# Kernel tuning notes

Measured on AMD Instinct MI355X. Metric: run time of the kernel, lower is better.

## Reference

```python
import jax, jax.numpy as jnp
import numpy as np

B, S, D, H = 2, 2048, 768, 12
HD = D // H
WINDOW = 64  # local_attention // 2
ROPE_THETA = 10000.0
NEG = -1e9


def setup_inputs() -> dict:
    key = jax.random.key(0)
    k1, k2, k3 = jax.random.split(key, 3)
    hidden_states = jax.random.normal(k1, (B, S, D), dtype=jnp.float32)
    Wqkv_w = jax.random.normal(k2, (3 * D, D), dtype=jnp.float32) * (D ** -0.5)
    Wo_w = jax.random.normal(k3, (D, D), dtype=jnp.float32) * (D ** -0.5)
    position_ids = jnp.broadcast_to(jnp.arange(S, dtype=jnp.int64 if jax.config.jax_enable_x64 else jnp.int32), (B, S))
    # additive sliding-window mask: 0 inside window, -1e9 outside (matches torch ModernBert mask construction)
    idx = np.arange(S)
    dist = np.abs(idx[:, None] - idx[None, :])
    sliding_window_mask = jnp.asarray(np.where(dist <= WINDOW, 0.0, NEG), dtype=jnp.float32)[None, None]  # [1,1,S,S]
    return {"hidden_states": hidden_states, "Wqkv_w": Wqkv_w, "Wo_w": Wo_w,
            "sliding_window_mask": sliding_window_mask, "position_ids": position_ids}


def _rotate_half(x):
    x1, x2 = jnp.split(x, 2, axis=-1)
    return jnp.concatenate([-x2, x1], axis=-1)


def reference(hidden_states, Wqkv_w, Wo_w, sliding_window_mask, position_ids):
    b, s, d = hidden_states.shape
    qkv = hidden_states @ Wqkv_w.T                      # [B,S,3D]
    qkv = qkv.reshape(b, s, 3, H, HD)
    q = qkv[:, :, 0].transpose(0, 2, 1, 3)              # [B,H,S,HD]
    k = qkv[:, :, 1].transpose(0, 2, 1, 3)
    v = qkv[:, :, 2].transpose(0, 2, 1, 3)
    # RoPE
    inv_freq = 1.0 / (ROPE_THETA ** (jnp.arange(0, HD, 2, dtype=jnp.float32) / HD))  # [HD/2]
    freqs = position_ids.astype(jnp.float32)[..., None] * inv_freq                   # [B,S,HD/2]
    emb = jnp.concatenate([freqs, freqs], axis=-1)                                   # [B,S,HD]
    cos = jnp.cos(emb)[:, None]                          # [B,1,S,HD]
    sin = jnp.sin(emb)[:, None]
    q = q * cos + _rotate_half(q) * sin
    k = k * cos + _rotate_half(k) * sin
    scale = HD ** -0.5
    scores = jnp.einsum('bhqd,bhkd->bhqk', q, k) * scale + sliding_window_mask       # [B,H,S,S]
    attn = jax.nn.softmax(scores.astype(jnp.float32), axis=-1).astype(q.dtype)
    out = jnp.einsum('bhqk,bhkd->bhqd', attn, v)         # [B,H,S,HD]
    out = out.transpose(0, 2, 1, 3).reshape(b, s, d)     # [B,S,D]
    return out @ Wo_w.T
```

## Files before the change

### kernel.cpp

```cpp
#include <hip/hip_runtime.h>
#include <hip/hip_bf16.h>
#include <cmath>

#define B_   2
#define S_   2048
#define D_   768
#define H_   12
#define HD_  64
#define WIN_ 64

typedef __bf16 bf16x8 __attribute__((ext_vector_type(8)));
typedef __bf16 bf16x4 __attribute__((ext_vector_type(4)));
typedef float  f32x4  __attribute__((ext_vector_type(4)));
typedef unsigned int u32;

__device__ __forceinline__ void async_ld16(const void* g, void* l) {
    __builtin_amdgcn_global_load_lds(
        (__attribute__((address_space(1))) void*)(size_t)g,
        (__attribute__((address_space(3))) void*)(u32)(size_t)l,
        16, 0, 0);
}

#define NHS (B_ * S_ * D_)
#define NWQ (3 * D_ * D_)
#define NWO (D_ * D_)

__global__ __launch_bounds__(256) void to_bf16_3(const float* __restrict__ a,
                                                 const float* __restrict__ b,
                                                 const float* __restrict__ c,
                                                 __bf16* __restrict__ oa,
                                                 __bf16* __restrict__ ob,
                                                 __bf16* __restrict__ oc) {
    const int NA = NHS / 4, NB = NWQ / 4;
    int v = blockIdx.x * 256 + threadIdx.x;
    const float* src; __bf16* dst; int idx;
    if (v < NA)           { src = a; dst = oa; idx = v; }
    else if (v < NA + NB) { src = b; dst = ob; idx = v - NA; }
    else                  { src = c; dst = oc; idx = v - NA - NB; }
    float4 x = ((const float4*)src)[idx];
    bf16x4 y = { (__bf16)x.x, (__bf16)x.y, (__bf16)x.z, (__bf16)x.w };
    *(bf16x4*)(dst + (size_t)idx * 4) = y;
}

#define BM 128
#define BN 128
#define BK 32

template <int MODE>
__global__ __launch_bounds__(256) void gemm_as(const __bf16* __restrict__ A,
                                               const __bf16* __restrict__ Bw,
                                               float* __restrict__ C,
                                               __bf16* __restrict__ qkv,
                                               __bf16* __restrict__ vt,
                                               int M, int N, int K) {
    __shared__ __attribute__((aligned(16))) __bf16 As[BM * BK];
    __shared__ __attribute__((aligned(16))) __bf16 Bs[BN * BK];

    const int tid  = threadIdx.x;
    const int m0   = blockIdx.y * BM;
    const int n0   = blockIdx.x * BN;
    const int w    = tid >> 6;
    const int lane = tid & 63;
    const int wm   = (w >> 1) * 64;
    const int wn   = (w & 1) * 64;
    const int fr   = lane & 15;
    const int fq   = lane >> 4;

    f32x4 acc[4][4] = {};

    for (int k0 = 0; k0 < K; k0 += BK) {
        #pragma unroll
        for (int i = 0; i < 2; ++i) {
            int c = i * 256 + tid;
            int row = c >> 2, cc = c & 3;
            async_ld16(A  + (size_t)(m0 + row) * K + k0 + cc * 8, As + c * 8);
            async_ld16(Bw + (size_t)(n0 + row) * K + k0 + cc * 8, Bs + c * 8);
        }
        __syncthreads();

        bf16x8 af[4], bfv[4];
        #pragma unroll
        for (int t = 0; t < 4; ++t) {
            af[t]  = *(const bf16x8*)(As + (wm + t * 16 + fr) * BK + fq * 8);
            bfv[t] = *(const bf16x8*)(Bs + (wn + t * 16 + fr) * BK + fq * 8);
        }
        #pragma unroll
        for (int ti = 0; ti < 4; ++ti)
            #pragma unroll
            for (int tj = 0; tj < 4; ++tj)
                acc[ti][tj] = __builtin_amdgcn_mfma_f32_16x16x32_bf16(
                    af[ti], bfv[tj], acc[ti][tj], 0, 0, 0);

        __syncthreads();
    }

    if (MODE == 0) {
        #pragma unroll
        for (int ti = 0; ti < 4; ++ti)
            #pragma unroll
            for (int tj = 0; tj < 4; ++tj) {
                const int col = n0 + wn + tj * 16 + fr;
                #pragma unroll
                for (int r = 0; r < 4; ++r) {
                    const int row = m0 + wm + ti * 16 + fq * 4 + r;
                    C[(size_t)row * N + col] = acc[ti][tj][r];
                }
            }
    } else {
        if (n0 < 2 * D_) {
            #pragma unroll
            for (int ti = 0; ti < 4; ++ti)
                #pragma unroll
                for (int tj = 0; tj < 4; ++tj) {
                    const int col = n0 + wn + tj * 16 + fr;
                    #pragma unroll
                    for (int r = 0; r < 4; ++r) {
                        const int row = m0 + wm + ti * 16 + fq * 4 + r;
                        qkv[(size_t)row * (2 * D_) + col] = (__bf16)acc[ti][tj][r];
                    }
                }
        } else {
            #pragma unroll
            for (int ti = 0; ti < 4; ++ti)
                #pragma unroll
                for (int tj = 0; tj < 4; ++tj) {
                    const int col = n0 + wn + tj * 16 + fr - 2 * D_;
                    const int h = col >> 6, d = col & 63;
                    const int row0 = m0 + wm + ti * 16 + fq * 4;
                    const int bb = row0 >> 11, t0 = row0 & (S_ - 1);
                    bf16x4 pk = { (__bf16)acc[ti][tj][0], (__bf16)acc[ti][tj][1],
                                  (__bf16)acc[ti][tj][2], (__bf16)acc[ti][tj][3] };
                    *(bf16x4*)(vt + ((size_t)((bb * H_ + h) * HD_ + d)) * S_ + t0) = pk;
                }
        }
    }
}

__global__ __launch_bounds__(256) void rope_bf(__bf16* __restrict__ qkv,
                                               const int* __restrict__ pos_ids) {
    int idx = blockIdx.x * 256 + threadIdx.x;
    const int d = idx & 31;
    const int h = (idx >> 5) % H_;
    const int m = idx / (32 * H_);

    const float pos = (float)pos_ids[m];
    const float inv_freq = __powf(10000.0f, -(float)d * (1.0f / 32.0f));
    float s, c;
    sincosf(pos * inv_freq, &s, &c);

    __bf16* qp = qkv + (size_t)m * (2 * D_) + h * HD_ + d;
    const float q1 = (float)qp[0], q2 = (float)qp[32];
    qp[0]  = (__bf16)(q1 * c - q2 * s);
    qp[32] = (__bf16)(q2 * c + q1 * s);

    __bf16* kp = qp + D_;
    const float k1 = (float)kp[0], k2 = (float)kp[32];
    kp[0]  = (__bf16)(k1 * c - k2 * s);
    kp[32] = (__bf16)(k2 * c + k1 * s);
}

__global__ __launch_bounds__(256) void attn_mfma(const __bf16* __restrict__ qkv,
                                                 const __bf16* __restrict__ vt,
                                                 __bf16* __restrict__ outb) {
    __shared__ __attribute__((aligned(16))) __bf16 smem[28672];
    __bf16* Qs  = smem;
    __bf16* Ks  = smem + 4096;
    __bf16* Vts = smem + 16384;

    const int i0  = blockIdx.x * 64;
    const int h   = blockIdx.y;
    const int b   = blockIdx.z;
    const int tid = threadIdx.x;
    const int w = tid >> 6, lane = tid & 63;
    const int fr = lane & 15, fq = lane >> 4;
    const int wq0 = w * 16;

    const size_t qrow0 = ((size_t)b * S_ + i0) * (2 * D_) + h * HD_;
    #pragma unroll
    for (int i = 0; i < 2; ++i) {
        int c = i * 256 + tid;
        int cc = c & 3, row = (c >> 2) & 63, ks = c >> 8;
        async_ld16(qkv + qrow0 + (size_t)row * (2 * D_) + ks * 32 + cc * 8,
                   Qs + c * 8);
    }
    #pragma unroll
    for (int i = 0; i < 6; ++i) {
        int c = i * 256 + tid;
        int ks = (i >= 3);
        int rem = c - ks * 768;
        int cc = rem & 3, row = rem >> 2;
        int j = i0 - 64 + row; j = min(max(j, 0), S_ - 1);
        async_ld16(qkv + ((size_t)b * S_ + j) * (2 * D_) + D_ + h * HD_ + ks * 32 + cc * 8,
                   Ks + c * 8);
    }
    const size_t vbase = (size_t)((b * H_ + h) * HD_) * S_;
    #pragma unroll
    for (int i = 0; i < 6; ++i) {
        int c = i * 256 + tid;
        int ks = c >> 8, rem = c & 255, d = rem >> 2, cc = rem & 3;
        int key = i0 - 64 + ks * 32 + cc * 8;
        key = min(max(key, 0), S_ - 8);
        async_ld16(vt + vbase + (size_t)d * S_ + key, Vts + c * 8);
    }
    __syncthreads();

    bf16x8 aq[2];
    aq[0] = *(const bf16x8*)(Qs + (0 * 64 + wq0 + fr) * 32 + fq * 8);
    aq[1] = *(const bf16x8*)(Qs + (1 * 64 + wq0 + fr) * 32 + fq * 8);

    f32x4 sc[12] = {};
    #pragma unroll
    for (int nt = 0; nt < 12; ++nt) {
        #pragma unroll
        for (int ks = 0; ks < 2; ++ks) {
            bf16x8 bk = *(const bf16x8*)(Ks + (ks * 192 + nt * 16 + fr) * 32 + fq * 8);
            sc[nt] = __builtin_amdgcn_mfma_f32_16x16x32_bf16(aq[ks], bk, sc[nt], 0, 0, 0);
        }
    }

    float mx[4] = { -1e30f, -1e30f, -1e30f, -1e30f };
    #pragma unroll
    for (int nt = 0; nt < 12; ++nt) {
        const int jr = nt * 16 + fr;
        const int j  = i0 - 64 + jr;
        const bool jv = (j >= 0) && (j < S_);
        #pragma unroll
        for (int r = 0; r < 4; ++r) {
            const int ir = wq0 + fq * 4 + r + 64;
            const int dd = ir - jr;
            const bool v = jv && (dd <= WIN_) && (dd >= -WIN_);
            sc[nt][r] = v ? sc[nt][r] * 0.125f : -1e30f;
            mx[r] = fmaxf(mx[r], sc[nt][r]);
        }
    }
    #pragma unroll
    for (int r = 0; r < 4; ++r)
        #pragma unroll
        for (int off = 1; off < 16; off <<= 1)
            mx[r] = fmaxf(mx[r], __shfl_xor(mx[r], off, 64));

    float sm[4] = { 0.f, 0.f, 0.f, 0.f };
    #pragma unroll
    for (int nt = 0; nt < 12; ++nt)
        #pragma unroll
        for (int r = 0; r < 4; ++r) {
            float e = __expf(sc[nt][r] - mx[r]);
            sc[nt][r] = e;
            sm[r] += e;
        }
    #pragma unroll
    for (int r = 0; r < 4; ++r) {
        #pragma unroll
        for (int off = 1; off < 16; off <<= 1)
            sm[r] += __shfl_xor(sm[r], off, 64);
        sm[r] = 1.0f / sm[r];
    }

    __syncthreads();

    __bf16* Pw = Ks + w * 3072;
    #pragma unroll
    for (int nt = 0; nt < 12; ++nt) {
        const int ks = nt >> 1, kk = (nt & 1) * 16 + fr;
        #pragma unroll
        for (int r = 0; r < 4; ++r)
            Pw[(ks * 16 + fq * 4 + r) * 32 + kk] = (__bf16)(sc[nt][r] * sm[r]);
    }

    f32x4 oacc[4] = {};
    #pragma unroll
    for (int ks = 0; ks < 6; ++ks) {
        bf16x8 ap = *(const bf16x8*)(Pw + (ks * 16 + fr) * 32 + fq * 8);
        #pragma unroll
        for (int nt2 = 0; nt2 < 4; ++nt2) {
            bf16x8 bv = *(const bf16x8*)(Vts + (ks * 64 + nt2 * 16 + fr) * 32 + fq * 8);
            oacc[nt2] = __builtin_amdgcn_mfma_f32_16x16x32_bf16(ap, bv, oacc[nt2], 0, 0, 0);
        }
    }

    const size_t obase = ((size_t)b * S_ + i0 + wq0) * D_ + h * HD_;
    #pragma unroll
    for (int nt2 = 0; nt2 < 4; ++nt2)
        #pragma unroll
        for (int r = 0; r < 4; ++r)
            outb[obase + (size_t)(fq * 4 + r) * D_ + nt2 * 16 + fr] = (__bf16)oacc[nt2][r];
}

extern "C" void kernel_launch(void* const* d_in, const int* in_sizes, int n_in,
                              void* d_out, int out_size, void* d_ws, size_t ws_size,
                              hipStream_t stream) {
    const float* hs   = (const float*)d_in[0];
    const float* wqkv = (const float*)d_in[1];
    const float* wo   = (const float*)d_in[2];
    const int*   pos  = (const int*)d_in[4];
    float* out = (float*)d_out;

    __bf16* base    = (__bf16*)d_ws;
    __bf16* hs_bf   = base;
    __bf16* wqkv_bf = hs_bf + NHS;
    __bf16* wo_bf   = wqkv_bf + NWQ;
    __bf16* qkv     = wo_bf + NWO;
    __bf16* vt      = qkv + (size_t)(B_ * S_) * (2 * D_);
    __bf16* attn_bf = vt + (size_t)B_ * H_ * HD_ * S_;

    to_bf16_3<<<(NHS + NWQ + NWO) / 1024, 256, 0, stream>>>(
        hs, wqkv, wo, hs_bf, wqkv_bf, wo_bf);

    gemm_as<1><<<dim3((3 * D_) / BN, (B_ * S_) / BM), 256, 0, stream>>>(
        hs_bf, wqkv_bf, nullptr, qkv, vt, B_ * S_, 3 * D_, D_);

    rope_bf<<<(B_ * S_ * H_ * 32) / 256, 256, 0, stream>>>(qkv, pos);

    attn_mfma<<<dim3(S_ / 64, H_, B_), 256, 0, stream>>>(qkv, vt, attn_bf);

    gemm_as<0><<<dim3(D_ / BN, (B_ * S_) / BM), 256, 0, stream>>>(
        attn_bf, wo_bf, out, nullptr, nullptr, B_ * S_, D_, D_);
}
```

Baseline: 161.9 us.

## Fuse RoPE into QKV GEMM epilogue, double GEMM K-tile, load Q directly

The separate RoPE kernel is removed. Rotation is now applied in the QKV GEMM epilogue on fp32 accumulators, pairing column tiles tj and tj+2 (d and d+32 within each 64-wide head), which saves a full read-modify-write pass over Q and K and one launch. The GEMM K-tile grows from 32 to 64, halving the number of barrier iterations at the cost of doubled LDS per block. The attention kernel now loads Q fragments straight from global memory into registers instead of staging them through LDS, which shrinks shared memory. Each thread computes sincos for its rows redundantly in the epilogue, and rounding changes slightly because RoPE is applied before the bf16 conversion.

```diff
diff --git a/kernel.cpp b/kernel.cpp
--- a/kernel.cpp
+++ b/kernel.cpp
@@ -44,7 +44,7 @@
 
 #define BM 128
 #define BN 128
-#define BK 32
+#define BK 64
 
 template <int MODE>
 __global__ __launch_bounds__(256) void gemm_as(const __bf16* __restrict__ A,
@@ -52,6 +52,7 @@
                                                float* __restrict__ C,
                                                __bf16* __restrict__ qkv,
                                                __bf16* __restrict__ vt,
+                                               const int* __restrict__ pos,
                                                int M, int N, int K) {
     __shared__ __attribute__((aligned(16))) __bf16 As[BM * BK];
     __shared__ __attribute__((aligned(16))) __bf16 Bs[BN * BK];
@@ -70,27 +71,29 @@
 
     for (int k0 = 0; k0 < K; k0 += BK) {
         #pragma unroll
-        for (int i = 0; i < 2; ++i) {
+        for (int i = 0; i < 4; ++i) {
             int c = i * 256 + tid;
-            int row = c >> 2, cc = c & 3;
+            int row = c >> 3, cc = c & 7;
             async_ld16(A  + (size_t)(m0 + row) * K + k0 + cc * 8, As + c * 8);
             async_ld16(Bw + (size_t)(n0 + row) * K + k0 + cc * 8, Bs + c * 8);
         }
         __syncthreads();
 
-        bf16x8 af[4], bfv[4];
-        #pragma unroll
-        for (int t = 0; t < 4; ++t) {
-            af[t]  = *(const bf16x8*)(As + (wm + t * 16 + fr) * BK + fq * 8);
-            bfv[t] = *(const bf16x8*)(Bs + (wn + t * 16 + fr) * BK + fq * 8);
-        }
-        #pragma unroll
-        for (int ti = 0; ti < 4; ++ti)
-            #pragma unroll
-            for (int tj = 0; tj < 4; ++tj)
-                acc[ti][tj] = __builtin_amdgcn_mfma_f32_16x16x32_bf16(
-                    af[ti], bfv[tj], acc[ti][tj], 0, 0, 0);
-
+        #pragma unroll
+        for (int ks = 0; ks < 2; ++ks) {
+            bf16x8 af[4], bfv[4];
+            #pragma unroll
+            for (int t = 0; t < 4; ++t) {
+                af[t]  = *(const bf16x8*)(As + (wm + t * 16 + fr) * BK + ks * 32 + fq * 8);
+                bfv[t] = *(const bf16x8*)(Bs + (wn + t * 16 + fr) * BK + ks * 32 + fq * 8);
+            }
+            #pragma unroll
+            for (int ti = 0; ti < 4; ++ti)
+                #pragma unroll
+                for (int tj = 0; tj < 4; ++tj)
+                    acc[ti][tj] = __builtin_amdgcn_mfma_f32_16x16x32_bf16(
+                        af[ti], bfv[tj], acc[ti][tj], 0, 0, 0);
+        }
         __syncthreads();
     }
 
@@ -108,6 +111,24 @@
             }
     } else {
         if (n0 < 2 * D_) {
+            const float invf0 = __powf(10000.0f, -(float)fr * (1.0f / 32.0f));
+            const float invf1 = __powf(10000.0f, -(float)(16 + fr) * (1.0f / 32.0f));
+            #pragma unroll
+            for (int ti = 0; ti < 4; ++ti)
+                #pragma unroll
+                for (int r = 0; r < 4; ++r) {
+                    const int row = m0 + wm + ti * 16 + fq * 4 + r;
+                    const float p = (float)pos[row];
+                    float s0, c0, s1, c1;
+                    sincosf(p * invf0, &s0, &c0);
+                    sincosf(p * invf1, &s1, &c1);
+                    const float a0 = acc[ti][0][r], a1 = acc[ti][2][r];
+                    acc[ti][0][r] = a0 * c0 - a1 * s0;
+                    acc[ti][2][r] = a1 * c0 + a0 * s0;
+                    const float b0 = acc[ti][1][r], b1 = acc[ti][3][r];
+                    acc[ti][1][r] = b0 * c1 - b1 * s1;
+                    acc[ti][3][r] = b1 * c1 + b0 * s1;
+                }
             #pragma unroll
             for (int ti = 0; ti < 4; ++ti)
                 #pragma unroll
@@ -136,36 +157,12 @@
     }
 }
 
-__global__ __launch_bounds__(256) void rope_bf(__bf16* __restrict__ qkv,
-                                               const int* __restrict__ pos_ids) {
-    int idx = blockIdx.x * 256 + threadIdx.x;
-    const int d = idx & 31;
-    const int h = (idx >> 5) % H_;
-    const int m = idx / (32 * H_);
-
-    const float pos = (float)pos_ids[m];
-    const float inv_freq = __powf(10000.0f, -(float)d * (1.0f / 32.0f));
-    float s, c;
-    sincosf(pos * inv_freq, &s, &c);
-
-    __bf16* qp = qkv + (size_t)m * (2 * D_) + h * HD_ + d;
-    const float q1 = (float)qp[0], q2 = (float)qp[32];
-    qp[0]  = (__bf16)(q1 * c - q2 * s);
-    qp[32] = (__bf16)(q2 * c + q1 * s);
-
-    __bf16* kp = qp + D_;
-    const float k1 = (float)kp[0], k2 = (float)kp[32];
-    kp[0]  = (__bf16)(k1 * c - k2 * s);
-    kp[32] = (__bf16)(k2 * c + k1 * s);
-}
-
 __global__ __launch_bounds__(256) void attn_mfma(const __bf16* __restrict__ qkv,
                                                  const __bf16* __restrict__ vt,
                                                  __bf16* __restrict__ outb) {
-    __shared__ __attribute__((aligned(16))) __bf16 smem[28672];
-    __bf16* Qs  = smem;
-    __bf16* Ks  = smem + 4096;
-    __bf16* Vts = smem + 16384;
+    __shared__ __attribute__((aligned(16))) __bf16 smem[24576];
+    __bf16* Ks  = smem;
+    __bf16* Vts = smem + 12288;
 
     const int i0  = blockIdx.x * 64;
     const int h   = blockIdx.y;
@@ -175,14 +172,6 @@
     const int fr = lane & 15, fq = lane >> 4;
     const int wq0 = w * 16;
 
-    const size_t qrow0 = ((size_t)b * S_ + i0) * (2 * D_) + h * HD_;
-    #pragma unroll
-    for (int i = 0; i < 2; ++i) {
-        int c = i * 256 + tid;
-        int cc = c & 3, row = (c >> 2) & 63, ks = c >> 8;
-        async_ld16(qkv + qrow0 + (size_t)row * (2 * D_) + ks * 32 + cc * 8,
-                   Qs + c * 8);
-    }
     #pragma unroll
     for (int i = 0; i < 6; ++i) {
         int c = i * 256 + tid;
@@ -202,11 +191,13 @@
         key = min(max(key, 0), S_ - 8);
         async_ld16(vt + vbase + (size_t)d * S_ + key, Vts + c * 8);
     }
+
+    const size_t qrow = ((size_t)b * S_ + i0 + wq0 + fr) * (2 * D_) + h * HD_;
+    bf16x8 aq[2];
+    aq[0] = *(const bf16x8*)(qkv + qrow + fq * 8);
+    aq[1] = *(const bf16x8*)(qkv + qrow + 32 + fq * 8);
+
     __syncthreads();
-
-    bf16x8 aq[2];
-    aq[0] = *(const bf16x8*)(Qs + (0 * 64 + wq0 + fr) * 32 + fq * 8);
-    aq[1] = *(const bf16x8*)(Qs + (1 * 64 + wq0 + fr) * 32 + fq * 8);
 
     f32x4 sc[12] = {};
     #pragma unroll
@@ -307,12 +298,10 @@
         hs, wqkv, wo, hs_bf, wqkv_bf, wo_bf);
 
     gemm_as<1><<<dim3((3 * D_) / BN, (B_ * S_) / BM), 256, 0, stream>>>(
-        hs_bf, wqkv_bf, nullptr, qkv, vt, B_ * S_, 3 * D_, D_);
-
-    rope_bf<<<(B_ * S_ * H_ * 32) / 256, 256, 0, stream>>>(qkv, pos);
+        hs_bf, wqkv_bf, nullptr, qkv, vt, pos, B_ * S_, 3 * D_, D_);
 
     attn_mfma<<<dim3(S_ / 64, H_, B_), 256, 0, stream>>>(qkv, vt, attn_bf);
 
     gemm_as<0><<<dim3(D_ / BN, (B_ * S_) / BM), 256, 0, stream>>>(
-        attn_bf, wo_bf, out, nullptr, nullptr, B_ * S_, D_, D_);
-}
+        attn_bf, wo_bf, out, nullptr, nullptr, nullptr, B_ * S_, D_, D_);
+}
```

After: 178.9 us. 1.11x slower.
